# Optimization experiments

Measured on AMD Instinct MI355X. Metric: run time of the kernel, lower is better.

The kernel has to match this reference:

```python
import jax, jax.numpy as jnp
import numpy as np

N = 100000   # nodes
E = 1600000  # edges (avg degree 16)
H = 4        # heads
D = 32       # per-head dim (= output_dim)
IN = 32      # input_dim (== output_dim for residual)
NEG_SLOPE = 0.2  # DGL GATConv leaky_relu default


def setup_inputs() -> dict:
    key = jax.random.key(0)
    ks = jax.random.split(key, 9)
    h = jax.random.normal(ks[0], (N, IN), jnp.float32)
    src = jax.random.randint(ks[1], (E,), 0, N, jnp.int32)
    dst = jax.random.randint(ks[2], (E,), 0, N, jnp.int32)
    W_fc = jax.random.normal(ks[3], (IN, H * D), jnp.float32) / np.sqrt(IN).astype(np.float32)
    attn_l = jax.random.normal(ks[4], (H, D), jnp.float32) * 0.1
    attn_r = jax.random.normal(ks[5], (H, D), jnp.float32) * 0.1
    bias_gat = jnp.zeros((H * D,), jnp.float32)
    W_out = jax.random.normal(ks[6], (H * D, D), jnp.float32) / np.sqrt(H * D).astype(np.float32)
    b_out = jnp.zeros((D,), jnp.float32)
    return {"h": h, "src": src, "dst": dst, "W_fc": W_fc, "attn_l": attn_l,
            "attn_r": attn_r, "bias_gat": bias_gat, "W_out": W_out, "b_out": b_out}


def reference(h, src, dst, W_fc, attn_l, attn_r, bias_gat, W_out, b_out):
    # GATConv: linear projection to [N, H, D]
    feat = (h @ W_fc).reshape(N, H, D)
    el = jnp.einsum('nhd,hd->nh', feat, attn_l)  # [N,H]
    er = jnp.einsum('nhd,hd->nh', feat, attn_r)  # [N,H]
    # per-edge unnormalized score, leaky relu
    e = el[src] + er[dst]                         # [E,H]
    e = jnp.where(e > 0, e, NEG_SLOPE * e)
    # segment softmax over edges grouped by destination node
    emax = jax.ops.segment_max(e, dst, num_segments=N)            # [N,H]
    ex = jnp.exp(e - emax[dst])                                   # [E,H]
    denom = jax.ops.segment_sum(ex, dst, num_segments=N)         # [N,H]
    alpha = ex / jnp.maximum(denom[dst], 1e-9)                    # [E,H]
    # attention-weighted scatter-add aggregation
    msg = feat[src] * alpha[:, :, None]                           # [E,H,D]
    rst = jax.ops.segment_sum(msg, dst, num_segments=N)          # [N,H,D]
    rst = rst.reshape(N, H * D) + bias_gat
    # out projection + ELU activation + residual
    out = rst @ W_out + b_out
    out = jnp.where(out > 0, out, jnp.expm1(out))  # ELU(alpha=1)
    return h + out
```

## Files before the change

### kernel.cpp

```cpp
#include <hip/hip_runtime.h>
#include <hip/hip_bf16.h>

#define NNODE 100000
#define NEDGE 1600000
#define NBLK_SCAN 98
#define KPH_BLOCKS 1564
#define QINT4 100000
#define FLAGBIT 0x80000000u

#if __has_builtin(__builtin_amdgcn_cvt_pk_fp8_f32) && __has_builtin(__builtin_amdgcn_cvt_pk_f32_fp8)
#define HAVE_FP8CVT 1
typedef float floatx2 __attribute__((ext_vector_type(2)));
#endif

#ifndef HAVE_FP8CVT
static __device__ __forceinline__ uint32_t fp8_enc1(float x) {
    uint32_t b = __float_as_uint(x);
    uint32_t s = (b >> 24) & 0x80u;
    float ax = fabsf(x);
    if (ax >= 448.f) return s | 0x7Eu;
    if (ax < 0.015625f) {
        uint32_t m = (uint32_t)__float2int_rn(ax * 512.f);
        if (m > 7u) return s | (1u << 3);
        return s | m;
    }
    uint32_t mag = b & 0x7fffffffu;
    mag += 0x7ffffu + ((mag >> 20) & 1u);
    int e8 = (int)(mag >> 23) - 120;
    if (e8 > 15) return s | 0x7Eu;
    return s | ((uint32_t)e8 << 3) | ((mag >> 20) & 7u);
}
static __device__ __forceinline__ float fp8_dec1(uint32_t v) {
    uint32_t s = (v & 0x80u) << 24;
    uint32_t e = (v >> 3) & 0xFu, m = v & 7u;
    uint32_t bits;
    if (e) bits = s | ((e + 120u) << 23) | (m << 20);
    else bits = m ? (s | (__float_as_uint((float)m) - (9u << 23))) : s;
    return __uint_as_float(bits);
}
#endif

static __device__ __forceinline__ unsigned short enc_fp8x2(float a, float b) {
#ifdef HAVE_FP8CVT
    return (unsigned short)(__builtin_amdgcn_cvt_pk_fp8_f32(a, b, 0, false) & 0xffff);
#else
    return (unsigned short)(fp8_enc1(a) | (fp8_enc1(b) << 8));
#endif
}
static __device__ __forceinline__ float2 dec_fp8x2(uint32_t u) {
#ifdef HAVE_FP8CVT
    floatx2 v = __builtin_amdgcn_cvt_pk_f32_fp8((int)u, false);
    return make_float2(v.x, v.y);
#else
    return make_float2(fp8_dec1(u & 0xffu), fp8_dec1((u >> 8) & 0xffu));
#endif
}

static __device__ __forceinline__ uint32_t pack_bf16(float a, float b) {
    __hip_bfloat162 t = __float22bfloat162_rn(make_float2(a, b));
    return *(uint32_t*)&t;
}

__global__ __launch_bounds__(256) void k_proj_hist(
        const float* __restrict__ hin, const float* __restrict__ Wfc,
        const float* __restrict__ attn_l, const float* __restrict__ attn_r,
        unsigned short* __restrict__ fe8, float* __restrict__ el, float* __restrict__ er,
        const int* __restrict__ dst, int* __restrict__ cnt, int* __restrict__ pos) {
    int tid = threadIdx.x;
    int ei = blockIdx.x * 256 + tid;
    bool have = ei < NEDGE / 4;
    int4 d, p;
    int* cntp = nullptr;
    if (have) {
        unsigned part = (unsigned)ei / (unsigned)QINT4;
        cntp = cnt + part * NNODE;
        d = ((const int4*)dst)[ei];
        p.x = atomicAdd(&cntp[d.x], 1);
        p.y = atomicAdd(&cntp[d.y], 1);
        p.z = atomicAdd(&cntp[d.z], 1);
        p.w = atomicAdd(&cntp[d.w], 1);
    }
    int l = tid & 63;
    int w = tid >> 6;
    int nbase = blockIdx.x * 64 + w * 16;
    int c0 = l * 2;
    float2 wreg[32];
#pragma unroll
    for (int k = 0; k < 32; k++)
        wreg[k] = *(const float2*)&Wfc[k * 128 + c0];
    float al0 = attn_l[c0], al1 = attn_l[c0 + 1];
    float ar0 = attn_r[c0], ar1 = attn_r[c0 + 1];
#pragma unroll 4
    for (int i = 0; i < 16; i++) {
        int n = nbase + i;
        if (n >= NNODE) break;
        float4 hv[8];
#pragma unroll
        for (int j = 0; j < 8; j++)
            hv[j] = *(const float4*)&hin[n * 32 + j * 4];
        float a0 = 0.f, a1 = 0.f;
#pragma unroll
        for (int j = 0; j < 8; j++) {
            a0 = fmaf(hv[j].x, wreg[j * 4 + 0].x, a0); a1 = fmaf(hv[j].x, wreg[j * 4 + 0].y, a1);
            a0 = fmaf(hv[j].y, wreg[j * 4 + 1].x, a0); a1 = fmaf(hv[j].y, wreg[j * 4 + 1].y, a1);
            a0 = fmaf(hv[j].z, wreg[j * 4 + 2].x, a0); a1 = fmaf(hv[j].z, wreg[j * 4 + 2].y, a1);
            a0 = fmaf(hv[j].w, wreg[j * 4 + 3].x, a0); a1 = fmaf(hv[j].w, wreg[j * 4 + 3].y, a1);
        }
        float ep = a0 * al0 + a1 * al1;
        float rp = a0 * ar0 + a1 * ar1;
#pragma unroll
        for (int m = 8; m; m >>= 1) {
            ep += __shfl_xor(ep, m);
            rp += __shfl_xor(rp, m);
        }
        if ((l & 15) == 0) {
            el[n * 4 + (l >> 4)] = ep;
            er[n * 4 + (l >> 4)] = rp;
        }
        fe8[(size_t)n * 64 + l] = enc_fp8x2(a0, a1);
    }
    if (have) ((int4*)pos)[ei] = p;
}

__global__ __launch_bounds__(256) void k_scan(
        const int* __restrict__ cnt, unsigned* __restrict__ word,
        int* __restrict__ offa, int* __restrict__ pb) {
    __shared__ int s[256];
    __shared__ int sBase;
    int t = threadIdx.x;
    int b = blockIdx.x;
    int base = b * 1024 + t * 4;
    int vA[4], vB[4], vC[4], v[4];
#pragma unroll
    for (int i = 0; i < 4; i++) {
        int n = base + i;
        if (n < NNODE) {
            int a = cnt[n], bb = cnt[NNODE + n], c = cnt[2 * NNODE + n], dd = cnt[3 * NNODE + n];
            vA[i] = a; vB[i] = bb; vC[i] = c;
            v[i] = a + bb + c + dd;
        } else { vA[i] = vB[i] = vC[i] = 0; v[i] = 0; }
    }
    int sum = v[0] + v[1] + v[2] + v[3];
    s[t] = sum;
    __syncthreads();
    for (int d = 1; d < 256; d <<= 1) {
        int x = (t >= d) ? s[t - d] : 0;
        __syncthreads();
        s[t] += x;
        __syncthreads();
    }
    int excl = s[t] - sum;
    if (t == 255)
        __hip_atomic_store(&word[b], (unsigned)s[255] | FLAGBIT,
                           __ATOMIC_RELEASE, __HIP_MEMORY_SCOPE_AGENT);
    if (t < 64) {
        unsigned acc = 0;
        for (int i = t; i < b; i += 64) {
            unsigned wv;
            do {
                wv = __hip_atomic_load(&word[i], __ATOMIC_ACQUIRE, __HIP_MEMORY_SCOPE_AGENT);
            } while (!(wv & FLAGBIT));
            acc += wv & ~FLAGBIT;
        }
#pragma unroll
        for (int o = 32; o; o >>= 1) acc += __shfl_down(acc, o);
        if (t == 0) sBase = (int)acc;
    }
    __syncthreads();
    int o0 = sBase + excl;
#pragma unroll
    for (int i = 0; i < 4; i++) {
        int n = base + i;
        if (n < NNODE) {
            offa[n] = o0;
            pb[n] = o0;
            pb[NNODE + n] = o0 + vA[i];
            pb[2 * NNODE + n] = o0 + vA[i] + vB[i];
            pb[3 * NNODE + n] = o0 + vA[i] + vB[i] + vC[i];
            o0 += v[i];
        }
    }
    if (b == NBLK_SCAN - 1 && t == 255) offa[NNODE] = NEDGE;
}

__global__ __launch_bounds__(256) void k_scatter(const int* __restrict__ src,
                                                 const int* __restrict__ dst,
                                                 const int* __restrict__ pos,
                                                 const int* __restrict__ pb,
                                                 int* __restrict__ ssrc) {
    int i = blockIdx.x * 256 + threadIdx.x;
    if (i >= NEDGE / 4) return;
    unsigned part = (unsigned)i / (unsigned)QINT4;
    const int* pbp = pb + part * NNODE;
    int4 s = ((const int4*)src)[i];
    int4 d = ((const int4*)dst)[i];
    int4 p = ((const int4*)pos)[i];
    int o0 = pbp[d.x];
    int o1 = pbp[d.y];
    int o2 = pbp[d.z];
    int o3 = pbp[d.w];
    ssrc[o0 + p.x] = s.x;
    ssrc[o1 + p.y] = s.y;
    ssrc[o2 + p.z] = s.z;
    ssrc[o3 + p.w] = s.w;
}

#define NPB 4
__global__ __launch_bounds__(256) void k_gather(
        const int* __restrict__ off, const int* __restrict__ ssrc,
        const float* __restrict__ el, const float* __restrict__ er,
        const unsigned short* __restrict__ fe8, const float* __restrict__ bias_gat,
        const float* __restrict__ Wout, const float* __restrict__ b_out,
        const float* __restrict__ hin, float* __restrict__ out) {
    __shared__ uint32_t sWu[2048];
    __shared__ __align__(8) uint2 sSE[NPB][4][64];
    __shared__ float sv[NPB][128];
    int tid = threadIdx.x;
    for (int i = tid; i < 2048; i += 256) {
        int ccp = i >> 5, jj = i & 31;
        sWu[i] = pack_bf16(Wout[(2 * ccp) * 32 + jj], Wout[(2 * ccp + 1) * 32 + jj]);
    }
    __syncthreads();
    int w = tid >> 6;
    int l = tid & 63;
    int n = blockIdx.x * NPB + w;
    int c0 = l * 2;
    int hh = l >> 4;
    float2 acc = make_float2(0.f, 0.f);
    float den = 0.f;
    int beg = off[n], end = off[n + 1];
    float4 erv = *(const float4*)&er[n * 4];

    for (int base = beg; base < end; base += 64) {
        int cnt = end - base; if (cnt > 64) cnt = 64;
        int s = 0;
        float4 e4 = make_float4(0.f, 0.f, 0.f, 0.f);
        if (l < cnt) {
            s = ssrc[base + l];
            float4 ev = *(const float4*)&el[s * 4];
            e4.x = ev.x + erv.x; e4.x = e4.x > 0.f ? e4.x : 0.2f * e4.x; e4.x = __expf(e4.x);
            e4.y = ev.y + erv.y; e4.y = e4.y > 0.f ? e4.y : 0.2f * e4.y; e4.y = __expf(e4.y);
            e4.z = ev.z + erv.z; e4.z = e4.z > 0.f ? e4.z : 0.2f * e4.z; e4.z = __expf(e4.z);
            e4.w = ev.w + erv.w; e4.w = e4.w > 0.f ? e4.w : 0.2f * e4.w; e4.w = __expf(e4.w);
        }
        int s0 = __shfl(s, 0);
        if (l >= cnt) s = s0;
        uint32_t uoff = (uint32_t)s * 64u;
        sSE[w][0][l] = make_uint2(uoff, __float_as_uint(e4.x));
        sSE[w][1][l] = make_uint2(uoff, __float_as_uint(e4.y));
        sSE[w][2][l] = make_uint2(uoff, __float_as_uint(e4.z));
        sSE[w][3][l] = make_uint2(uoff, __float_as_uint(e4.w));
        __builtin_amdgcn_wave_barrier();
        int rounds = (cnt + 7) >> 3;
        for (int r = 0; r < rounds; r++) {
            int e = r * 8;
            uint2 m[8]; uint32_t uu[8];
#pragma unroll
            for (int q = 0; q < 8; q++)
                m[q] = sSE[w][hh][e + q];
#pragma unroll
            for (int q = 0; q < 8; q++)
                uu[q] = fe8[m[q].x + (uint32_t)l];
#pragma unroll
            for (int q = 0; q < 8; q++) {
                float x = __uint_as_float(m[q].y);
                float2 f = dec_fp8x2(uu[q]);
                den += x;
                acc.x = fmaf(x, f.x, acc.x);
                acc.y = fmaf(x, f.y, acc.y);
            }
        }
        __builtin_amdgcn_wave_barrier();
    }
    float inv = 1.f / fmaxf(den, 1e-9f);
    float2 val;
    val.x = acc.x * inv + bias_gat[c0];
    val.y = acc.y * inv + bias_gat[c0 + 1];
    *(float2*)&sv[w][c0] = val;
    __builtin_amdgcn_wave_barrier();
    int j = l & 31, g2 = l >> 5;
    float p = 0.f;
    const float* vv = sv[w];
#pragma unroll 8
    for (int ccp = g2 * 32; ccp < g2 * 32 + 32; ccp++) {
        uint32_t u = sWu[ccp * 32 + j];
        p = fmaf(vv[2 * ccp],     __uint_as_float(u << 16),          p);
        p = fmaf(vv[2 * ccp + 1], __uint_as_float(u & 0xffff0000u), p);
    }
    p += __shfl_xor(p, 32);
    if (g2 == 0) {
        float a = p > 0.f ? p : expm1f(p);
        out[n * 32 + j] = hin[n * 32 + j] + a;
    }
}

extern "C" void kernel_launch(void* const* d_in, const int* in_sizes, int n_in,
                              void* d_out, int out_size, void* d_ws, size_t ws_size,
                              hipStream_t stream) {
    const float* hin      = (const float*)d_in[0];
    const int*   src      = (const int*)d_in[1];
    const int*   dst      = (const int*)d_in[2];
    const float* Wfc      = (const float*)d_in[3];
    const float* attn_l   = (const float*)d_in[4];
    const float* attn_r   = (const float*)d_in[5];
    const float* bias_gat = (const float*)d_in[6];
    const float* Wout     = (const float*)d_in[7];
    const float* b_out    = (const float*)d_in[8];
    float* out = (float*)d_out;

    char* ws = (char*)d_ws;
    size_t o = 0;
    unsigned short* fe8 = (unsigned short*)(ws + o); o += (size_t)NNODE * 64 * 2;
    o = (o + 15) & ~(size_t)15;
    float* el      = (float*)(ws + o);    o += (size_t)NNODE * 4 * 4;
    float* er      = (float*)(ws + o);    o += (size_t)NNODE * 4 * 4;
    int*   cnt     = (int*)(ws + o);      o += (size_t)4 * NNODE * 4;
    unsigned* word = (unsigned*)(ws + o); o += (size_t)NBLK_SCAN * 4;
    int*   offa    = (int*)(ws + o);      o += (size_t)(NNODE + 1) * 4;
    int*   pb      = (int*)(ws + o);      o += (size_t)4 * NNODE * 4;
    int*   pos     = (int*)(ws + o);      o += (size_t)NEDGE * 4;
    int*   ssrc    = (int*)(ws + o);      o += (size_t)NEDGE * 4;

    hipMemsetAsync(cnt, 0, (size_t)(4 * NNODE + NBLK_SCAN) * 4, stream);

    k_proj_hist<<<KPH_BLOCKS, 256, 0, stream>>>(
        hin, Wfc, attn_l, attn_r, fe8, el, er, dst, cnt, pos);
    k_scan<<<NBLK_SCAN, 256, 0, stream>>>(cnt, word, offa, pb);
    k_scatter<<<(NEDGE / 4 + 255) / 256, 256, 0, stream>>>(src, dst, pos, pb, ssrc);
    k_gather<<<NNODE / NPB, 256, 0, stream>>>(offa, ssrc, el, er, fe8, bias_gat,
                                              Wout, b_out, hin, out);
}
```

Baseline: 219.3 us.

## Gather 8 fp8 features per lane across 4 edges in parallel

```diff
diff --git a/kernel.cpp b/kernel.cpp
--- a/kernel.cpp
+++ b/kernel.cpp
@@ -47,12 +47,14 @@
     return (unsigned short)(fp8_enc1(a) | (fp8_enc1(b) << 8));
 #endif
 }
-static __device__ __forceinline__ float2 dec_fp8x2(uint32_t u) {
+template <bool HI>
+static __device__ __forceinline__ float2 dec_fp8x2_sel(uint32_t u) {
 #ifdef HAVE_FP8CVT
-    floatx2 v = __builtin_amdgcn_cvt_pk_f32_fp8((int)u, false);
+    floatx2 v = __builtin_amdgcn_cvt_pk_f32_fp8((int)u, HI);
     return make_float2(v.x, v.y);
 #else
-    return make_float2(fp8_dec1(u & 0xffu), fp8_dec1((u >> 8) & 0xffu));
+    uint32_t w = HI ? (u >> 16) : u;
+    return make_float2(fp8_dec1(w & 0xffu), fp8_dec1((w >> 8) & 0xffu));
 #endif
 }
 
@@ -224,9 +226,13 @@
     int w = tid >> 6;
     int l = tid & 63;
     int n = blockIdx.x * NPB + w;
-    int c0 = l * 2;
-    int hh = l >> 4;
-    float2 acc = make_float2(0.f, 0.f);
+    int lo = l & 15;
+    int g  = l >> 4;
+    int hq = lo >> 2;
+    const uint2* fe8q = (const uint2*)fe8;
+    float acc8[8];
+#pragma unroll
+    for (int i = 0; i < 8; i++) acc8[i] = 0.f;
     float den = 0.f;
     int beg = off[n], end = off[n + 1];
     float4 erv = *(const float4*)&er[n * 4];
@@ -245,38 +251,62 @@
         }
         int s0 = __shfl(s, 0);
         if (l >= cnt) s = s0;
-        uint32_t uoff = (uint32_t)s * 64u;
+        uint32_t uoff = (uint32_t)s * 16u;
         sSE[w][0][l] = make_uint2(uoff, __float_as_uint(e4.x));
         sSE[w][1][l] = make_uint2(uoff, __float_as_uint(e4.y));
         sSE[w][2][l] = make_uint2(uoff, __float_as_uint(e4.z));
         sSE[w][3][l] = make_uint2(uoff, __float_as_uint(e4.w));
         __builtin_amdgcn_wave_barrier();
-        int rounds = (cnt + 7) >> 3;
-        for (int r = 0; r < rounds; r++) {
-            int e = r * 8;
-            uint2 m[8]; uint32_t uu[8];
-#pragma unroll
-            for (int q = 0; q < 8; q++)
-                m[q] = sSE[w][hh][e + q];
-#pragma unroll
-            for (int q = 0; q < 8; q++)
-                uu[q] = fe8[m[q].x + (uint32_t)l];
-#pragma unroll
-            for (int q = 0; q < 8; q++) {
-                float x = __uint_as_float(m[q].y);
-                float2 f = dec_fp8x2(uu[q]);
+        int nquad = (cnt + 3) >> 2;
+        for (int t0 = 0; t0 < nquad; t0 += 4) {
+            uint2 m[4]; uint2 rq[4];
+#pragma unroll
+            for (int k = 0; k < 4; k++)
+                m[k] = sSE[w][hq][(t0 + k) * 4 + g];
+#pragma unroll
+            for (int k = 0; k < 4; k++)
+                rq[k] = fe8q[m[k].x + (uint32_t)lo];
+#pragma unroll
+            for (int k = 0; k < 4; k++) {
+                float x = __uint_as_float(m[k].y);
                 den += x;
-                acc.x = fmaf(x, f.x, acc.x);
-                acc.y = fmaf(x, f.y, acc.y);
+                float2 f0 = dec_fp8x2_sel<false>(rq[k].x);
+                float2 f1 = dec_fp8x2_sel<true>(rq[k].x);
+                float2 f2 = dec_fp8x2_sel<false>(rq[k].y);
+                float2 f3 = dec_fp8x2_sel<true>(rq[k].y);
+                acc8[0] = fmaf(x, f0.x, acc8[0]);
+                acc8[1] = fmaf(x, f0.y, acc8[1]);
+                acc8[2] = fmaf(x, f1.x, acc8[2]);
+                acc8[3] = fmaf(x, f1.y, acc8[3]);
+                acc8[4] = fmaf(x, f2.x, acc8[4]);
+                acc8[5] = fmaf(x, f2.y, acc8[5]);
+                acc8[6] = fmaf(x, f3.x, acc8[6]);
+                acc8[7] = fmaf(x, f3.y, acc8[7]);
             }
         }
         __builtin_amdgcn_wave_barrier();
     }
+#pragma unroll
+    for (int i = 0; i < 8; i++) {
+        acc8[i] += __shfl_xor(acc8[i], 16);
+        acc8[i] += __shfl_xor(acc8[i], 32);
+    }
+    den += __shfl_xor(den, 16);
+    den += __shfl_xor(den, 32);
     float inv = 1.f / fmaxf(den, 1e-9f);
-    float2 val;
-    val.x = acc.x * inv + bias_gat[c0];
-    val.y = acc.y * inv + bias_gat[c0 + 1];
-    *(float2*)&sv[w][c0] = val;
+    if (l < 16) {
+        float4 va, vb;
+        va.x = acc8[0] * inv + bias_gat[lo * 8 + 0];
+        va.y = acc8[1] * inv + bias_gat[lo * 8 + 1];
+        va.z = acc8[2] * inv + bias_gat[lo * 8 + 2];
+        va.w = acc8[3] * inv + bias_gat[lo * 8 + 3];
+        vb.x = acc8[4] * inv + bias_gat[lo * 8 + 4];
+        vb.y = acc8[5] * inv + bias_gat[lo * 8 + 5];
+        vb.z = acc8[6] * inv + bias_gat[lo * 8 + 6];
+        vb.w = acc8[7] * inv + bias_gat[lo * 8 + 7];
+        *(float4*)&sv[w][lo * 8]     = va;
+        *(float4*)&sv[w][lo * 8 + 4] = vb;
+    }
     __builtin_amdgcn_wave_barrier();
     int j = l & 31, g2 = l >> 5;
     float p = 0.f;
```

Measured after the change: 223.9 us. 2.1% more time.
